# Optimization experiments

Hardware: AMD Instinct MI355X
Metric: run time of the kernel (lower is better)

The kernel has to match this reference:

```python
import jax, jax.numpy as jnp
import numpy as np

B, T, D = 2, 4096, 1024          # batch, seq_len, d_model
L, H, F, K = 2, 16, 4096, 2048   # n_blocks, n_heads, d_ff, router top-k (T//2)
DH = D // H


def _ln(x, scale, bias):
    m = jnp.mean(x, -1, keepdims=True)
    v = jnp.var(x, -1, keepdims=True)
    return (x - m) * jax.lax.rsqrt(v + 1e-5) * scale + bias


def setup_inputs() -> dict:
    key = jax.random.key(0)
    ks = jax.random.split(key, 6)
    n = lambda k, sh, s: jax.random.normal(k, sh, jnp.float32) * s
    return {
        "x": n(ks[0], (B, T, D), 1.0),
        "w_router": n(ks[1], (D,), 0.02),
        "b_router": jnp.zeros((), jnp.float32),
        "ln1_scale": jnp.ones((L, D), jnp.float32),
        "ln1_bias": jnp.zeros((L, D), jnp.float32),
        "w_qkv": n(ks[2], (L, D, 3 * D), 0.02),
        "b_qkv": jnp.zeros((L, 3 * D), jnp.float32),
        "w_o": n(ks[3], (L, D, D), 0.02),
        "b_o": jnp.zeros((L, D), jnp.float32),
        "ln2_scale": jnp.ones((L, D), jnp.float32),
        "ln2_bias": jnp.zeros((L, D), jnp.float32),
        "w1": n(ks[4], (L, D, F), 0.02),
        "b1": jnp.zeros((L, F), jnp.float32),
        "w2": n(ks[5], (L, F, D), 0.02),
        "b2": jnp.zeros((L, D), jnp.float32),
    }


def reference(x, w_router, b_router, ln1_scale, ln1_bias, w_qkv, b_qkv,
              w_o, b_o, ln2_scale, ln2_bias, w1, b1, w2, b2):
    # 1. router scores all (active) tokens; prev_selected is None (first recursion step)
    logits = jnp.einsum('btd,d->bt', x, w_router) + b_router          # (B, T)
    # 2. expert-choice: top-K tokens by score
    _, idx = jax.lax.top_k(logits, K)                                  # (B, K)
    idx = jnp.sort(idx, axis=1)                                        # restore sequence order
    gate = jax.nn.sigmoid(jnp.take_along_axis(logits, idx, axis=1))[..., None]  # (B, K, 1)
    h = jnp.take_along_axis(x, idx[..., None], axis=1)                 # gather -> (B, K, D)
    # 3. shared transformer blocks on the gathered subsequence
    causal = jnp.tril(jnp.ones((K, K), bool))
    scale = 1.0 / np.sqrt(DH).astype(np.float32)
    for l in range(L):
        a = _ln(h, ln1_scale[l], ln1_bias[l])
        qkv = a @ w_qkv[l] + b_qkv[l]
        q, k_, v = jnp.split(qkv, 3, axis=-1)
        q = q.reshape(B, K, H, DH).transpose(0, 2, 1, 3)
        k_ = k_.reshape(B, K, H, DH).transpose(0, 2, 1, 3)
        v = v.reshape(B, K, H, DH).transpose(0, 2, 1, 3)
        s = jnp.einsum('bhqd,bhkd->bhqk', q, k_) * scale               # (B, H, K, K)
        s = jnp.where(causal, s, jnp.finfo(s.dtype).min)
        p = jax.nn.softmax(s, axis=-1)
        o = jnp.einsum('bhqk,bhkd->bhqd', p, v).transpose(0, 2, 1, 3).reshape(B, K, D)
        h = h + o @ w_o[l] + b_o[l]
        m = _ln(h, ln2_scale[l], ln2_bias[l])
        h = h + jax.nn.gelu(m @ w1[l] + b1[l]) @ w2[l] + b2[l]
    # 4. gate-weighted scatter-add back into the full hidden state
    h_out = h * gate
    total = x.at[jnp.arange(B)[:, None], idx].add(h_out)               # (B, T, D)
    return total, idx, logits
```

## Files before the change

### kernel.cpp

```cpp
#include <hip/hip_runtime.h>
#include <hip/hip_bf16.h>
#include <cstdint>

typedef unsigned short u16;
typedef __attribute__((ext_vector_type(8))) short s16x8;
typedef __attribute__((ext_vector_type(4))) float f32x4;
typedef __attribute__((ext_vector_type(4))) u16 u16x4;

constexpr int Bc = 2, Tc = 4096, Dc = 1024, Lc = 2, Hc = 16, Fc = 4096, Kc = 2048, DHc = 64;
constexpr int Mc = Bc * Kc;

__device__ __forceinline__ u16 f2b(float f) {
  __hip_bfloat16 h = __float2bfloat16(f);
  return *reinterpret_cast<u16*>(&h);
}

__device__ __forceinline__ float wred_sum(float v) {
#pragma unroll
  for (int m = 32; m >= 1; m >>= 1) v += __shfl_xor(v, m, 64);
  return v;
}

__device__ __forceinline__ void gl2lds16(const void* g, void* l) {
  __builtin_amdgcn_global_load_lds(
      (const __attribute__((address_space(1))) void*)(uintptr_t)g,
      (__attribute__((address_space(3))) void*)(uintptr_t)l, 16, 0, 0);
}

__global__ void transp_kernel(const float* __restrict__ in, u16* __restrict__ out, int R, int C) {
  __shared__ float t[32][33];
  int c0 = blockIdx.x * 32, r0 = blockIdx.y * 32;
  int tr = threadIdx.x >> 5, tc = threadIdx.x & 31;
#pragma unroll
  for (int i = 0; i < 4; i++)
    t[tr + i * 8][tc] = in[(size_t)(r0 + tr + i * 8) * C + c0 + tc];
  __syncthreads();
#pragma unroll
  for (int i = 0; i < 4; i++)
    out[(size_t)(c0 + tr + i * 8) * R + r0 + tc] = f2b(t[tc][tr + i * 8]);
}

__global__ void router_kernel(const float* __restrict__ x, const float* __restrict__ wr,
                              const float* __restrict__ br, float* __restrict__ out_lg,
                              float* __restrict__ ws_lg) {
  int tid = threadIdx.x, w = tid >> 6, l = tid & 63;
  int token = blockIdx.x * 4 + w;
  const float4* xr = (const float4*)(x + (size_t)token * Dc);
  const float4* wv = (const float4*)wr;
  float acc = 0.f;
#pragma unroll
  for (int i = 0; i < 4; i++) {
    float4 a = xr[l + i * 64], bw = wv[l + i * 64];
    acc += a.x * bw.x + a.y * bw.y + a.z * bw.z + a.w * bw.w;
  }
  acc = wred_sum(acc);
  if (l == 0) {
    float v = acc + br[0];
    out_lg[token] = v;
    ws_lg[token] = v;
  }
}

__global__ void topk_kernel(const float* __restrict__ logits, int* __restrict__ idxi,
                            float* __restrict__ gate, int* __restrict__ inv,
                            float* __restrict__ out_idx) {
  __shared__ float lg[Tc];
  __shared__ unsigned int key[Tc];
  __shared__ unsigned int hist[256];
  __shared__ unsigned int sscan[256];
  __shared__ unsigned int wsum[16], woff[16];
  __shared__ unsigned int sel_info[2];
  int b = blockIdx.x, tid = threadIdx.x;
#pragma unroll
  for (int j = 0; j < 4; j++) {
    int t = tid + j * 1024;
    float v = logits[b * Tc + t];
    lg[t] = v;
    unsigned int u = __float_as_uint(v);
    key[t] = (u & 0x80000000u) ? ~u : (u | 0x80000000u);
  }
  if (tid == 0) { sel_info[0] = 0u; sel_info[1] = (unsigned int)Kc; }
  __syncthreads();
  for (int pass = 0; pass < 4; ++pass) {
    int shift = 24 - 8 * pass;
    if (tid < 256) hist[tid] = 0u;
    __syncthreads();
    unsigned int prefix = sel_info[0];
#pragma unroll
    for (int j = 0; j < 4; j++) {
      unsigned int k = key[tid + j * 1024];
      if ((unsigned int)(((unsigned long long)k) >> (shift + 8)) == prefix)
        atomicAdd(&hist[(k >> shift) & 255u], 1u);
    }
    __syncthreads();
    if (tid < 256) sscan[tid] = hist[tid];
    __syncthreads();
    for (int s = 1; s < 256; s <<= 1) {
      unsigned int add = 0u;
      if (tid < 256 && tid + s < 256) add = sscan[tid + s];
      __syncthreads();
      if (tid < 256) sscan[tid] += add;
      __syncthreads();
    }
    if (tid < 256) {
      unsigned int above = sscan[tid] - hist[tid];
      unsigned int rem = sel_info[1];
      if (above < rem && sscan[tid] >= rem) {
        sel_info[0] = (prefix << 8) | (unsigned int)tid;
        sel_info[1] = rem - above;
      }
    }
    __syncthreads();
  }
  unsigned int thr = sel_info[0];
  unsigned int R = sel_info[1];
  int base = tid * 4;
  unsigned int sgt = 0, seq = 0;
#pragma unroll
  for (int j = 0; j < 4; j++) {
    unsigned int k = key[base + j];
    sgt += (k > thr); seq += (k == thr);
  }
  unsigned int pk = (sgt << 16) | seq;
  int lane = tid & 63, wid = tid >> 6;
  unsigned int inc = pk;
#pragma unroll
  for (int m = 1; m < 64; m <<= 1) {
    unsigned int o = __shfl_up(inc, m, 64);
    if (lane >= m) inc += o;
  }
  if (lane == 63) wsum[wid] = inc;
  __syncthreads();
  if (tid == 0) {
    unsigned int run = 0;
    for (int i2 = 0; i2 < 16; i2++) { woff[i2] = run; run += wsum[i2]; }
  }
  __syncthreads();
  unsigned int exc = inc - pk + woff[wid];
  unsigned int run_gt = exc >> 16, run_eq = exc & 0xFFFFu;
#pragma unroll
  for (int j = 0; j < 4; j++) {
    int t = base + j;
    unsigned int k = key[t];
    bool isgt = k > thr, iseq = (k == thr);
    bool selv = isgt || (iseq && run_eq < R);
    if (selv) {
      unsigned int pos = run_gt + (run_eq < R ? run_eq : R);
      idxi[b * Kc + pos] = t;
      out_idx[b * Kc + pos] = (float)t;
      gate[b * Kc + pos] = 1.f / (1.f + __expf(-lg[t]));
      inv[b * Tc + t] = (int)pos;
    } else {
      inv[b * Tc + t] = -1;
    }
    run_gt += isgt ? 1u : 0u;
    run_eq += iseq ? 1u : 0u;
  }
}

__global__ void gather_kernel(const float* __restrict__ x, const int* __restrict__ idxi,
                              float* __restrict__ h) {
  int blk = blockIdx.x, tid = threadIdx.x;
  int b = blk >> 11;
  int t = idxi[blk];
  ((float4*)(h + (size_t)blk * Dc))[tid] =
      ((const float4*)(x + ((size_t)b * Tc + t) * Dc))[tid];
}

__global__ void ln_kernel(const float* __restrict__ h, const float* __restrict__ sc,
                          const float* __restrict__ bi, u16* __restrict__ out) {
  __shared__ float red[8];
  int row = blockIdx.x, tid = threadIdx.x, w = tid >> 6, l = tid & 63;
  float4 v = ((const float4*)(h + (size_t)row * Dc))[tid];
  float s = v.x + v.y + v.z + v.w;
  float q = v.x * v.x + v.y * v.y + v.z * v.z + v.w * v.w;
  s = wred_sum(s);
  q = wred_sum(q);
  if (l == 0) { red[w] = s; red[w + 4] = q; }
  __syncthreads();
  s = red[0] + red[1] + red[2] + red[3];
  q = red[4] + red[5] + red[6] + red[7];
  float mean = s * (1.f / Dc);
  float var = q * (1.f / Dc) - mean * mean;
  float rsd = rsqrtf(var + 1e-5f);
  float4 scv = ((const float4*)sc)[tid];
  float4 biv = ((const float4*)bi)[tid];
  u16x4 o;
  o.x = f2b((v.x - mean) * rsd * scv.x + biv.x);
  o.y = f2b((v.y - mean) * rsd * scv.y + biv.y);
  o.z = f2b((v.z - mean) * rsd * scv.z + biv.z);
  o.w = f2b((v.w - mean) * rsd * scv.w + biv.w);
  *(u16x4*)(out + (size_t)row * Dc + tid * 4) = o;
}

template <int EPI>
__global__ __launch_bounds__(256) void gemm_bt(
    const u16* __restrict__ A, const u16* __restrict__ BT,
    const float* __restrict__ bias, int Kd, int kdchunk, int N, int gridN,
    float* __restrict__ outf, u16* __restrict__ outb,
    u16* __restrict__ qd, u16* __restrict__ kd, u16* __restrict__ vd) {
  __shared__ __align__(16) u16 lsA[2][128 * 32];
  __shared__ __align__(16) u16 lsB[2][128 * 32];
  int tid = threadIdx.x;
  int w = tid >> 6, l = tid & 63;
  int wu = __builtin_amdgcn_readfirstlane(w);
  int wr = w >> 1, wc = w & 1;
  int lr = l & 15, lg = l >> 4;
  int nwg = gridDim.x;
  int orig = blockIdx.x;
  int qq = nwg >> 3, rr = nwg & 7;
  int xcd = orig & 7;
  int wgid = (xcd < rr ? xcd * (qq + 1) : rr * (qq + 1) + (xcd - rr) * qq) + (orig >> 3);
  int bm = wgid / gridN, bn = wgid % gridN;
  int kz = blockIdx.z;
  int k0 = kz * kdchunk;
  int srow = tid >> 2, scol = (tid & 3) * 8;
  const u16* ga = A + (size_t)(bm * 128 + srow) * Kd + k0 + scol;
  const u16* gb = BT + (size_t)(bn * 128 + srow) * Kd + k0 + scol;

  auto stage = [&](int buf, int kt) {
    gl2lds16(ga + kt, &lsA[buf][wu * 512]);
    gl2lds16(ga + (size_t)64 * Kd + kt, &lsA[buf][2048 + wu * 512]);
    gl2lds16(gb + kt, &lsB[buf][wu * 512]);
    gl2lds16(gb + (size_t)64 * Kd + kt, &lsB[buf][2048 + wu * 512]);
  };

  f32x4 acc[4][4] = {};
  int nt = kdchunk >> 5;
  stage(0, 0);
  for (int t = 0; t < nt; ++t) {
    int cur = t & 1;
    if (t + 1 < nt) {
      stage(cur ^ 1, (t + 1) * 32);
      asm volatile("s_waitcnt vmcnt(4)" ::: "memory");
    } else {
      asm volatile("s_waitcnt vmcnt(0)" ::: "memory");
    }
    __builtin_amdgcn_s_barrier();
    asm volatile("" ::: "memory");
    s16x8 af[4], bf[4];
#pragma unroll
    for (int i = 0; i < 4; i++)
      af[i] = *(const s16x8*)&lsA[cur][(wr * 64 + i * 16 + lr) * 32 + lg * 8];
#pragma unroll
    for (int j = 0; j < 4; j++)
      bf[j] = *(const s16x8*)&lsB[cur][(wc * 64 + j * 16 + lr) * 32 + lg * 8];
#pragma unroll
    for (int i = 0; i < 4; i++)
#pragma unroll
      for (int j = 0; j < 4; j++)
        acc[i][j] = __builtin_amdgcn_mfma_f32_16x16x32_bf16(af[i], bf[j], acc[i][j], 0, 0, 0);
    asm volatile("" ::: "memory");
    __builtin_amdgcn_s_barrier();
  }
  int row0 = bm * 128 + wr * 64 + lg * 4;
  int col0 = bn * 128 + wc * 64 + lr;
  bool addb = (kz == 0);
#pragma unroll
  for (int i = 0; i < 4; i++) {
#pragma unroll
    for (int j = 0; j < 4; j++) {
      int col = col0 + j * 16;
      float bcol = addb ? bias[col] : 0.f;
#pragma unroll
      for (int r = 0; r < 4; r++) {
        int row = row0 + i * 16 + r;
        float v = acc[i][j][r] + bcol;
        if constexpr (EPI == 0) {
          int sec = col >> 10, n1 = col & 1023, hh = n1 >> 6, dh = n1 & 63;
          int b = row >> 11, kq = row & 2047;
          size_t bh = (size_t)(b * Hc + hh);
          if (sec == 0) {
            qd[(bh * Kc + kq) * DHc + dh] = f2b(v * 0.125f);
          } else if (sec == 1) {
            kd[(bh * Kc + kq) * DHc + dh] = f2b(v);
          } else {
            vd[(bh * DHc + dh) * Kc + kq] = f2b(v);
          }
        } else if constexpr (EPI == 1) {
          atomicAdd(&outf[(size_t)row * N + col], v);
        } else {
          float z = 0.7978845608028654f * (v + 0.044715f * v * v * v);
          float g = v / (1.f + __expf(-2.f * z));
          outb[(size_t)row * N + col] = f2b(g);
        }
      }
    }
  }
}

__global__ __launch_bounds__(256) void attn_fwd(const u16* __restrict__ Q,
                                                const u16* __restrict__ Kb,
                                                const u16* __restrict__ Vt,
                                                u16* __restrict__ O) {
  __shared__ __align__(16) u16 Kl[2][4096];
  __shared__ __align__(16) u16 Vl[2][4096];
  __shared__ __align__(16) u16 Pl[4][1024];
  int tid = threadIdx.x, w = tid >> 6, l = tid & 63;
  int lr = l & 15, lg = l >> 4;
  int bid = blockIdx.x;
  int qb = 31 - (bid >> 5);
  int bh = bid & 31;
  const u16* Qp = Q + (size_t)bh * Kc * DHc;
  const u16* Kp = Kb + (size_t)bh * Kc * DHc;
  const u16* Vp = Vt + (size_t)bh * DHc * Kc;
  int q0 = qb * 64 + w * 16;
  s16x8 qf0 = *(const s16x8*)(Qp + (size_t)(q0 + lr) * DHc + lg * 8);
  s16x8 qf1 = *(const s16x8*)(Qp + (size_t)(q0 + lr) * DHc + 32 + lg * 8);
  int skv = tid >> 2;
  int sc8 = (tid & 3) * 8;
  u16* pw = Pl[w];
  f32x4 oa[4] = {};
  float lsum[4] = {0.f, 0.f, 0.f, 0.f};

  auto stage = [&](int buf, int kv0) {
    const u16* kbase = Kp + (size_t)(kv0 + skv) * DHc + sc8;
    gl2lds16(kbase, &Kl[buf][w * 512]);
    gl2lds16(kbase + 32, &Kl[buf][2048 + w * 512]);
    const u16* vbase = Vp + (size_t)skv * Kc + kv0 + sc8;
    gl2lds16(vbase, &Vl[buf][w * 512]);
    gl2lds16(vbase + 32, &Vl[buf][2048 + w * 512]);
  };

  int nsteps = qb + 1;
  stage(0, 0);
  for (int t = 0; t < nsteps; ++t) {
    int cur = t & 1;
    int kv0 = t * 64;
    if (t + 1 < nsteps) {
      stage(cur ^ 1, kv0 + 64);
      asm volatile("s_waitcnt vmcnt(4)" ::: "memory");
    } else {
      asm volatile("s_waitcnt vmcnt(0)" ::: "memory");
    }
    __builtin_amdgcn_s_barrier();
    asm volatile("" ::: "memory");
    f32x4 s[4];
#pragma unroll
    for (int f = 0; f < 4; f++) {
      f32x4 z = {};
      z = __builtin_amdgcn_mfma_f32_16x16x32_bf16(
          qf0, *(const s16x8*)&Kl[cur][(f * 16 + lr) * 32 + lg * 8], z, 0, 0, 0);
      s[f] = __builtin_amdgcn_mfma_f32_16x16x32_bf16(
          qf1, *(const s16x8*)&Kl[cur][2048 + (f * 16 + lr) * 32 + lg * 8], z, 0, 0, 0);
    }
#pragma unroll
    for (int f = 0; f < 4; f++) {
      int kv = kv0 + f * 16 + lr;
#pragma unroll
      for (int r = 0; r < 4; r++) {
        int qrow = q0 + lg * 4 + r;
        float p = (kv <= qrow) ? __expf(s[f][r]) : 0.f;
        lsum[r] += p;
        pw[(f >> 1) * 512 + (lg * 4 + r) * 32 + (f & 1) * 16 + lr] = f2b(p);
      }
    }
#pragma unroll
    for (int ks = 0; ks < 2; ks++) {
      s16x8 pf = *(const s16x8*)&pw[ks * 512 + lr * 32 + lg * 8];
#pragma unroll
      for (int d4 = 0; d4 < 4; d4++)
        oa[d4] = __builtin_amdgcn_mfma_f32_16x16x32_bf16(
            pf, *(const s16x8*)&Vl[cur][ks * 2048 + (d4 * 16 + lr) * 32 + lg * 8],
            oa[d4], 0, 0, 0);
    }
    asm volatile("" ::: "memory");
    __builtin_amdgcn_s_barrier();
  }
#pragma unroll
  for (int msk = 1; msk < 16; msk <<= 1)
#pragma unroll
    for (int r = 0; r < 4; r++) lsum[r] += __shfl_xor(lsum[r], msk, 64);
  int b = bh >> 4, hh = bh & 15;
#pragma unroll
  for (int r = 0; r < 4; r++) {
    float invl = 1.f / lsum[r];
    int qrow = q0 + lg * 4 + r;
    u16* orow = O + ((size_t)(b * Kc + qrow) * Dc) + hh * DHc;
#pragma unroll
    for (int d4 = 0; d4 < 4; d4++)
      orow[d4 * 16 + lr] = f2b(oa[d4][r] * invl);
  }
}

__global__ void scatter_kernel(const float* __restrict__ x, const float* __restrict__ h,
                               const float* __restrict__ gate, const int* __restrict__ inv,
                               float* __restrict__ out) {
  int row = blockIdx.x, tid = threadIdx.x;
  int b = row >> 12;
  float4 xv = ((const float4*)(x + (size_t)row * Dc))[tid];
  int pos = inv[row];
  if (pos >= 0) {
    float g = gate[b * Kc + pos];
    float4 hv = ((const float4*)(h + (size_t)(b * Kc + pos) * Dc))[tid];
    xv.x += g * hv.x; xv.y += g * hv.y; xv.z += g * hv.z; xv.w += g * hv.w;
  }
  ((float4*)(out + (size_t)row * Dc))[tid] = xv;
}

extern "C" void kernel_launch(void* const* d_in, const int* in_sizes, int n_in,
                              void* d_out, int out_size, void* d_ws, size_t ws_size,
                              hipStream_t stream) {
  const float* x = (const float*)d_in[0];
  const float* w_router = (const float*)d_in[1];
  const float* b_router = (const float*)d_in[2];
  const float* ln1_s = (const float*)d_in[3];
  const float* ln1_b = (const float*)d_in[4];
  const float* w_qkv = (const float*)d_in[5];
  const float* b_qkv = (const float*)d_in[6];
  const float* w_o = (const float*)d_in[7];
  const float* b_o = (const float*)d_in[8];
  const float* ln2_s = (const float*)d_in[9];
  const float* ln2_b = (const float*)d_in[10];
  const float* w1 = (const float*)d_in[11];
  const float* b1 = (const float*)d_in[12];
  const float* w2 = (const float*)d_in[13];
  const float* b2 = (const float*)d_in[14];

  float* out_total = (float*)d_out;
  float* out_idx = out_total + (size_t)Bc * Tc * Dc;
  float* out_lg = out_idx + Bc * Kc;

  char* p = (char*)d_ws;
  auto carve = [&](size_t bytes) {
    char* r = p;
    p += (bytes + 255) & ~(size_t)255;
    return r;
  };
  float* lg_ws = (float*)carve((size_t)Bc * Tc * 4);
  int* idx_ws = (int*)carve((size_t)Bc * Kc * 4);
  float* gate_ws = (float*)carve((size_t)Bc * Kc * 4);
  int* inv_ws = (int*)carve((size_t)Bc * Tc * 4);
  float* h_ws = (float*)carve((size_t)Mc * Dc * 4);
  u16* a_bf = (u16*)carve((size_t)Mc * Dc * 2);
  u16* o_bf = (u16*)carve((size_t)Mc * Dc * 2);
  u16* g_bf = (u16*)carve((size_t)Mc * Fc * 2);
  u16* qbuf = (u16*)carve((size_t)Bc * Hc * Kc * DHc * 2);
  u16* kbuf = (u16*)carve((size_t)Bc * Hc * Kc * DHc * 2);
  u16* vtbuf = (u16*)carve((size_t)Bc * Hc * Kc * DHc * 2);
  u16* wqkvT = (u16*)carve((size_t)Lc * 3 * Dc * Dc * 2);
  u16* woT = (u16*)carve((size_t)Lc * Dc * Dc * 2);
  u16* w1T = (u16*)carve((size_t)Lc * Dc * Fc * 2);
  u16* w2T = (u16*)carve((size_t)Lc * Fc * Dc * 2);

  for (int l2 = 0; l2 < Lc; ++l2) {
    transp_kernel<<<dim3(3 * Dc / 32, Dc / 32), 256, 0, stream>>>(
        w_qkv + (size_t)l2 * Dc * 3 * Dc, wqkvT + (size_t)l2 * 3 * Dc * Dc, Dc, 3 * Dc);
    transp_kernel<<<dim3(Dc / 32, Dc / 32), 256, 0, stream>>>(
        w_o + (size_t)l2 * Dc * Dc, woT + (size_t)l2 * Dc * Dc, Dc, Dc);
    transp_kernel<<<dim3(Fc / 32, Dc / 32), 256, 0, stream>>>(
        w1 + (size_t)l2 * Dc * Fc, w1T + (size_t)l2 * Fc * Dc, Dc, Fc);
    transp_kernel<<<dim3(Dc / 32, Fc / 32), 256, 0, stream>>>(
        w2 + (size_t)l2 * Fc * Dc, w2T + (size_t)l2 * Dc * Fc, Fc, Dc);
  }
  router_kernel<<<Bc * Tc / 4, 256, 0, stream>>>(x, w_router, b_router, out_lg, lg_ws);
  topk_kernel<<<Bc, 1024, 0, stream>>>(lg_ws, idx_ws, gate_ws, inv_ws, out_idx);
  gather_kernel<<<Mc, 256, 0, stream>>>(x, idx_ws, h_ws);
  for (int l2 = 0; l2 < Lc; ++l2) {
    ln_kernel<<<Mc, 256, 0, stream>>>(h_ws, ln1_s + l2 * Dc, ln1_b + l2 * Dc, a_bf);
    gemm_bt<0><<<dim3((3 * Dc / 128) * (Mc / 128), 1, 1), 256, 0, stream>>>(
        a_bf, wqkvT + (size_t)l2 * 3 * Dc * Dc, b_qkv + l2 * 3 * Dc,
        Dc, Dc, 3 * Dc, 3 * Dc / 128, nullptr, nullptr, qbuf, kbuf, vtbuf);
    attn_fwd<<<Bc * Hc * (Kc / 64), 256, 0, stream>>>(qbuf, kbuf, vtbuf, o_bf);
    gemm_bt<1><<<dim3((Dc / 128) * (Mc / 128), 1, 2), 256, 0, stream>>>(
        o_bf, woT + (size_t)l2 * Dc * Dc, b_o + l2 * Dc,
        Dc, Dc / 2, Dc, Dc / 128, h_ws, nullptr, nullptr, nullptr, nullptr);
    ln_kernel<<<Mc, 256, 0, stream>>>(h_ws, ln2_s + l2 * Dc, ln2_b + l2 * Dc, a_bf);
    gemm_bt<2><<<dim3((Fc / 128) * (Mc / 128), 1, 1), 256, 0, stream>>>(
        a_bf, w1T + (size_t)l2 * Fc * Dc, b1 + l2 * Fc,
        Dc, Dc, Fc, Fc / 128, nullptr, g_bf, nullptr, nullptr, nullptr);
    gemm_bt<1><<<dim3((Dc / 128) * (Mc / 128), 1, 4), 256, 0, stream>>>(
        g_bf, w2T + (size_t)l2 * Dc * Fc, b2 + l2 * Dc,
        Fc, Fc / 4, Dc, Dc / 128, h_ws, nullptr, nullptr, nullptr, nullptr);
  }
  scatter_kernel<<<Bc * Tc, 256, 0, stream>>>(x, h_ws, gate_ws, inv_ws, out_total);
}
```

Baseline: 746.3 us.

## Enlarge GEMM tiles to 256x256 with 512 threads and 4-stage LDS pipeline

The bf16 GEMM kernel now uses 256x256 output tiles with 8 waves of 128x64 each. It replaces the double buffer with a 4-deep LDS ring that prefetches three K-steps ahead, dropping the trailing barrier per iteration. The output-projection GEMM split-K goes from 2 to 4 chunks. The aim is more operand reuse and better latency hiding, at the cost of 128 KB of LDS, higher register pressure, and fewer workgroups per GEMM, which may underfill the CUs.

```diff
diff --git a/kernel.cpp b/kernel.cpp
--- a/kernel.cpp
+++ b/kernel.cpp
@@ -194,17 +194,17 @@
 }
 
 template <int EPI>
-__global__ __launch_bounds__(256) void gemm_bt(
+__global__ __launch_bounds__(512) void gemm_bt(
     const u16* __restrict__ A, const u16* __restrict__ BT,
     const float* __restrict__ bias, int Kd, int kdchunk, int N, int gridN,
     float* __restrict__ outf, u16* __restrict__ outb,
     u16* __restrict__ qd, u16* __restrict__ kd, u16* __restrict__ vd) {
-  __shared__ __align__(16) u16 lsA[2][128 * 32];
-  __shared__ __align__(16) u16 lsB[2][128 * 32];
+  __shared__ __align__(16) u16 lsA[4][256 * 32];
+  __shared__ __align__(16) u16 lsB[4][256 * 32];
   int tid = threadIdx.x;
   int w = tid >> 6, l = tid & 63;
   int wu = __builtin_amdgcn_readfirstlane(w);
-  int wr = w >> 1, wc = w & 1;
+  int wr = w >> 2, wc = w & 3;
   int lr = l & 15, lg = l >> 4;
   int nwg = gridDim.x;
   int orig = blockIdx.x;
@@ -215,49 +215,48 @@
   int kz = blockIdx.z;
   int k0 = kz * kdchunk;
   int srow = tid >> 2, scol = (tid & 3) * 8;
-  const u16* ga = A + (size_t)(bm * 128 + srow) * Kd + k0 + scol;
-  const u16* gb = BT + (size_t)(bn * 128 + srow) * Kd + k0 + scol;
-
-  auto stage = [&](int buf, int kt) {
+  const u16* ga = A + (size_t)(bm * 256 + srow) * Kd + k0 + scol;
+  const u16* gb = BT + (size_t)(bn * 256 + srow) * Kd + k0 + scol;
+
+  auto stage = [&](int buf, int t) {
+    int kt = t * 32;
     gl2lds16(ga + kt, &lsA[buf][wu * 512]);
-    gl2lds16(ga + (size_t)64 * Kd + kt, &lsA[buf][2048 + wu * 512]);
+    gl2lds16(ga + (size_t)128 * Kd + kt, &lsA[buf][4096 + wu * 512]);
     gl2lds16(gb + kt, &lsB[buf][wu * 512]);
-    gl2lds16(gb + (size_t)64 * Kd + kt, &lsB[buf][2048 + wu * 512]);
+    gl2lds16(gb + (size_t)128 * Kd + kt, &lsB[buf][4096 + wu * 512]);
   };
 
-  f32x4 acc[4][4] = {};
+  f32x4 acc[8][4] = {};
   int nt = kdchunk >> 5;
   stage(0, 0);
+  if (nt > 1) stage(1, 1);
+  if (nt > 2) stage(2, 2);
   for (int t = 0; t < nt; ++t) {
-    int cur = t & 1;
-    if (t + 1 < nt) {
-      stage(cur ^ 1, (t + 1) * 32);
-      asm volatile("s_waitcnt vmcnt(4)" ::: "memory");
-    } else {
-      asm volatile("s_waitcnt vmcnt(0)" ::: "memory");
-    }
+    int cur = t & 3;
+    if (t + 2 < nt)      asm volatile("s_waitcnt vmcnt(8)" ::: "memory");
+    else if (t + 1 < nt) asm volatile("s_waitcnt vmcnt(4)" ::: "memory");
+    else                 asm volatile("s_waitcnt vmcnt(0)" ::: "memory");
     __builtin_amdgcn_s_barrier();
     asm volatile("" ::: "memory");
-    s16x8 af[4], bf[4];
-#pragma unroll
-    for (int i = 0; i < 4; i++)
-      af[i] = *(const s16x8*)&lsA[cur][(wr * 64 + i * 16 + lr) * 32 + lg * 8];
+    if (t + 3 < nt) stage((t + 3) & 3, t + 3);
+    s16x8 bfr[4];
 #pragma unroll
     for (int j = 0; j < 4; j++)
-      bf[j] = *(const s16x8*)&lsB[cur][(wc * 64 + j * 16 + lr) * 32 + lg * 8];
-#pragma unroll
-    for (int i = 0; i < 4; i++)
+      bfr[j] = *(const s16x8*)&lsB[cur][(wc * 64 + j * 16 + lr) * 32 + lg * 8];
+#pragma unroll
+    for (int i = 0; i < 8; i++) {
+      s16x8 afr = *(const s16x8*)&lsA[cur][(wr * 128 + i * 16 + lr) * 32 + lg * 8];
 #pragma unroll
       for (int j = 0; j < 4; j++)
-        acc[i][j] = __builtin_amdgcn_mfma_f32_16x16x32_bf16(af[i], bf[j], acc[i][j], 0, 0, 0);
+        acc[i][j] = __builtin_amdgcn_mfma_f32_16x16x32_bf16(afr, bfr[j], acc[i][j], 0, 0, 0);
+    }
     asm volatile("" ::: "memory");
-    __builtin_amdgcn_s_barrier();
-  }
-  int row0 = bm * 128 + wr * 64 + lg * 4;
-  int col0 = bn * 128 + wc * 64 + lr;
+  }
+  int row0 = bm * 256 + wr * 128 + lg * 4;
+  int col0 = bn * 256 + wc * 64 + lr;
   bool addb = (kz == 0);
 #pragma unroll
-  for (int i = 0; i < 4; i++) {
+  for (int i = 0; i < 8; i++) {
 #pragma unroll
     for (int j = 0; j < 4; j++) {
       int col = col0 + j * 16;
@@ -458,20 +457,20 @@
   gather_kernel<<<Mc, 256, 0, stream>>>(x, idx_ws, h_ws);
   for (int l2 = 0; l2 < Lc; ++l2) {
     ln_kernel<<<Mc, 256, 0, stream>>>(h_ws, ln1_s + l2 * Dc, ln1_b + l2 * Dc, a_bf);
-    gemm_bt<0><<<dim3((3 * Dc / 128) * (Mc / 128), 1, 1), 256, 0, stream>>>(
+    gemm_bt<0><<<dim3((Mc / 256) * (3 * Dc / 256), 1, 1), 512, 0, stream>>>(
         a_bf, wqkvT + (size_t)l2 * 3 * Dc * Dc, b_qkv + l2 * 3 * Dc,
-        Dc, Dc, 3 * Dc, 3 * Dc / 128, nullptr, nullptr, qbuf, kbuf, vtbuf);
+        Dc, Dc, 3 * Dc, 3 * Dc / 256, nullptr, nullptr, qbuf, kbuf, vtbuf);
     attn_fwd<<<Bc * Hc * (Kc / 64), 256, 0, stream>>>(qbuf, kbuf, vtbuf, o_bf);
-    gemm_bt<1><<<dim3((Dc / 128) * (Mc / 128), 1, 2), 256, 0, stream>>>(
+    gemm_bt<1><<<dim3((Mc / 256) * (Dc / 256), 1, 4), 512, 0, stream>>>(
         o_bf, woT + (size_t)l2 * Dc * Dc, b_o + l2 * Dc,
-        Dc, Dc / 2, Dc, Dc / 128, h_ws, nullptr, nullptr, nullptr, nullptr);
+        Dc, Dc / 4, Dc, Dc / 256, h_ws, nullptr, nullptr, nullptr, nullptr);
     ln_kernel<<<Mc, 256, 0, stream>>>(h_ws, ln2_s + l2 * Dc, ln2_b + l2 * Dc, a_bf);
-    gemm_bt<2><<<dim3((Fc / 128) * (Mc / 128), 1, 1), 256, 0, stream>>>(
+    gemm_bt<2><<<dim3((Mc / 256) * (Fc / 256), 1, 1), 512, 0, stream>>>(
         a_bf, w1T + (size_t)l2 * Fc * Dc, b1 + l2 * Fc,
-        Dc, Dc, Fc, Fc / 128, nullptr, g_bf, nullptr, nullptr, nullptr);
-    gemm_bt<1><<<dim3((Dc / 128) * (Mc / 128), 1, 4), 256, 0, stream>>>(
+        Dc, Dc, Fc, Fc / 256, nullptr, g_bf, nullptr, nullptr, nullptr);
+    gemm_bt<1><<<dim3((Mc / 256) * (Dc / 256), 1, 4), 512, 0, stream>>>(
         g_bf, w2T + (size_t)l2 * Dc * Fc, b2 + l2 * Dc,
-        Fc, Fc / 4, Dc, Dc / 128, h_ws, nullptr, nullptr, nullptr, nullptr);
+        Fc, Fc / 4, Dc, Dc / 256, h_ws, nullptr, nullptr, nullptr, nullptr);
   }
   scatter_kernel<<<Bc * Tc, 256, 0, stream>>>(x, h_ws, gate_ws, inv_ws, out_total);
 }
```

After: 831.0 us. 1.11x slower.
